# Kernel tuning notes

Hardware: AMD Instinct MI355X
Metric: run time of the kernel (lower is better)

## Reference

```python
import math
import jax, jax.numpy as jnp
import numpy as np

N_HEADS = 16


def setup_inputs() -> dict:
    key = jax.random.key(0)
    k1, k2 = jax.random.split(key)
    # qkv: [N, H*C, T] queries; y: [N, H*C, S] keys/values (k = v = y)
    qkv = jax.random.normal(k1, (2, 1024, 2048), dtype=jnp.float32)
    y = jax.random.normal(k2, (2, 1024, 2048), dtype=jnp.float32)
    return {"qkv": qkv, "y": y}


def reference(qkv, y):
    bs, width, length = qkv.shape
    ch = width // N_HEADS  # head dim = 64
    q = qkv.reshape(bs * N_HEADS, ch, length)          # [B*H, C, T]
    k = v = y.reshape(bs * N_HEADS, ch, -1)            # [B*H, C, S]
    scale = 1.0 / math.sqrt(math.sqrt(ch))             # applied to both q and k
    weight = jnp.einsum('bct,bcs->bts', q * scale, k * scale)  # [B*H, T, S]
    weight = jax.nn.softmax(weight.astype(jnp.float32), axis=-1).astype(weight.dtype)
    a = jnp.einsum('bts,bcs->bct', weight, v)          # [B*H, C, T]
    return a.reshape(bs, -1, length)                   # [N, H*C, T]
```

## Files before the change

kernel.cpp:

```cpp
#include <hip/hip_runtime.h>
#include <hip/hip_bf16.h>


typedef __attribute__((ext_vector_type(4))) float f32x4;
typedef __attribute__((ext_vector_type(8))) short bf16x8;
typedef __attribute__((ext_vector_type(4))) float float4_t;
typedef __attribute__((ext_vector_type(4))) unsigned u32x4;

__device__ __forceinline__ unsigned short f2bf(float f) {
  unsigned u = __builtin_bit_cast(unsigned, f);
  u += 0x7FFFu + ((u >> 16) & 1u);
  return (unsigned short)(u >> 16);
}

__device__ __forceinline__ float exp2_fast(float x) {
  float r;
  asm("v_exp_f32 %0, %1" : "=v"(r) : "v"(x));
  return r;
}

__device__ __forceinline__ unsigned cvt_pk_bf16(float a, float b) {
  unsigned r;
  asm("v_cvt_pk_bf16_f32 %0, %1, %2" : "=v"(r) : "v"(a), "v"(b));
  return r;
}

#define GLOAD_LDS16(g, l) __builtin_amdgcn_global_load_lds(                 \
    (const __attribute__((address_space(1))) unsigned*)(g),                 \
    (__attribute__((address_space(3))) unsigned*)(l), 16, 0, 0)

#define SCL (0.35355339059327373f * 1.2011224087864498f)

__global__ __launch_bounds__(256)
void prep(const float* __restrict__ qkv, const float* __restrict__ y,
          unsigned short* __restrict__ kT, unsigned short* __restrict__ v,
          unsigned short* __restrict__ qT) {
  __shared__ unsigned short tb[64][66];
  const int tid = threadIdx.x;
  const int isQ = blockIdx.x >> 10;
  const int b2  = blockIdx.x & 1023;
  const int bh  = b2 >> 5;
  const int s0  = (b2 & 31) * 64;
  const float* src = (isQ ? qkv : y) + (size_t)bh * 131072;

  const int c = tid >> 2, j = tid & 3;
  float fv[16];
  #pragma unroll
  for (int p = 0; p < 4; ++p) {
    float4_t a = *(const float4_t*)(src + c * 2048 + s0 + j * 16 + p * 4);
    #pragma unroll
    for (int i = 0; i < 4; ++i) fv[p * 4 + i] = a[i];
  }
  if (!isQ) {
    bf16x8 u0, u1;
    #pragma unroll
    for (int i = 0; i < 8; ++i) { u0[i] = (short)f2bf(fv[i]); u1[i] = (short)f2bf(fv[8 + i]); }
    unsigned short* vp = v + (size_t)bh * 131072 + c * 2048 + s0 + j * 16;
    *(bf16x8*)(vp) = u0;
    *(bf16x8*)(vp + 8) = u1;
  }
  #pragma unroll
  for (int m = 0; m < 8; ++m) {
    unsigned lo = f2bf(fv[2 * m] * SCL);
    unsigned hi = f2bf(fv[2 * m + 1] * SCL);
    *(unsigned*)&tb[c][j * 16 + 2 * m] = lo | (hi << 16);
  }
  __syncthreads();

  const int srow = tid >> 2, i2 = tid & 3;
  unsigned short outv[16];
  #pragma unroll
  for (int m = 0; m < 16; ++m) outv[m] = tb[i2 * 16 + m][srow];
  unsigned short* dT = (isQ ? qT : kT) + (size_t)bh * 131072 +
                       (size_t)(s0 + srow) * 64 + i2 * 16;
  *(bf16x8*)(dT)     = *(bf16x8*)&outv[0];
  *(bf16x8*)(dT + 8) = *(bf16x8*)&outv[8];
}

#define WBS 32768

__global__ __launch_bounds__(512, 2)
void attn_main(const unsigned short* __restrict__ kT,
               const unsigned short* __restrict__ v,
               const unsigned short* __restrict__ qT,
               float* __restrict__ out) {
  __shared__ __align__(16) char smem[2 * WBS];
  const int tid  = threadIdx.x;
  const int lane = tid & 63;
  const int w    = tid >> 6;
  const int c15  = lane & 15;
  const int g    = lane >> 4;

  const int bid = blockIdx.x;
  const int bh  = (bid & 7) * 4 + ((bid >> 3) & 3);
  const int t0  = (bid >> 5) * 256;

  const unsigned short* kg = kT + (size_t)bh * 131072;
  const unsigned short* vg = v  + (size_t)bh * 131072;
  float*                og = out + (size_t)bh * 131072;

  bf16x8 qf[2][2];
  {
    const unsigned short* qp0 = qT + (size_t)bh * 131072 +
                                (size_t)(t0 + w * 32 + c15) * 64 + 8 * g;
    qf[0][0] = *(const bf16x8*)(qp0);
    qf[0][1] = *(const bf16x8*)(qp0 + 32);
    qf[1][0] = *(const bf16x8*)(qp0 + 1024);
    qf[1][1] = *(const bf16x8*)(qp0 + 1024 + 32);
  }

  const int sr = tid >> 3, sb = tid & 7;
  const int ss = sb ^ (sr & 7);
  const unsigned short* kbase = kg + sr * 64 + ss * 8;
  const unsigned short* vbase = vg + sr * 2048 + ss * 8;
  char* const slds = smem + tid * 16;

  f32x4 oacc[2][4];
  #pragma unroll
  for (int tg = 0; tg < 2; ++tg)
    #pragma unroll
    for (int nc = 0; nc < 4; ++nc) oacc[tg][nc] = (f32x4){0.f, 0.f, 0.f, 0.f};
  float lsum[2] = {0.f, 0.f};

  auto QK = [&](f32x4 (&acc)[2][4], char* kb) {
    #pragma unroll
    for (int kt = 0; kt < 2; ++kt)
      #pragma unroll
      for (int nt = 0; nt < 4; ++nt) {
        const int srow = nt * 16 + c15;
        bf16x8 kf = *(bf16x8*)(kb + srow * 128 + (((kt * 4 + g) ^ (srow & 7)) * 16));
        acc[0][nt] = __builtin_amdgcn_mfma_f32_16x16x32_bf16(kf, qf[0][kt], acc[0][nt], 0, 0, 0);
        acc[1][nt] = __builtin_amdgcn_mfma_f32_16x16x32_bf16(kf, qf[1][kt], acc[1][nt], 0, 0, 0);
      }
  };
  auto SM = [&](f32x4 (&acc)[2][4], bf16x8 (&pa)[2][2]) {
    #pragma unroll
    for (int tg = 0; tg < 2; ++tg) {
      unsigned W[8];
      #pragma unroll
      for (int nt = 0; nt < 4; ++nt) {
        float p0 = exp2_fast(acc[tg][nt][0]);
        float p1 = exp2_fast(acc[tg][nt][1]);
        float p2 = exp2_fast(acc[tg][nt][2]);
        float p3 = exp2_fast(acc[tg][nt][3]);
        lsum[tg] += (p0 + p1) + (p2 + p3);
        W[nt * 2]     = cvt_pk_bf16(p0, p1);
        W[nt * 2 + 1] = cvt_pk_bf16(p2, p3);
      }
      #pragma unroll
      for (int kt = 0; kt < 2; ++kt) {
        unsigned a0 = W[kt * 4 + 0], b0 = W[kt * 4 + 2];
        unsigned a1 = W[kt * 4 + 1], b1 = W[kt * 4 + 3];
        asm volatile("v_permlane32_swap_b32 %0, %1" : "+v"(a0), "+v"(b0));
        asm volatile("v_permlane32_swap_b32 %0, %1" : "+v"(a1), "+v"(b1));
        asm volatile("v_permlane16_swap_b32 %0, %1" : "+v"(a0), "+v"(b0));
        asm volatile("v_permlane16_swap_b32 %0, %1" : "+v"(a1), "+v"(b1));
        u32x4 fw = {a0, a1, b0, b1};
        pa[tg][kt] = __builtin_bit_cast(bf16x8, fw);
      }
    }
  };
  auto PV = [&](bf16x8 (&pa)[2][2], char* vb) {
    #pragma unroll
    for (int kt = 0; kt < 2; ++kt)
      #pragma unroll
      for (int nc = 0; nc < 4; ++nc) {
        const int crow = nc * 16 + c15;
        bf16x8 vf = *(bf16x8*)(vb + crow * 128 + (((kt * 4 + g) ^ (crow & 7)) * 16));
        oacc[0][nc] = __builtin_amdgcn_mfma_f32_16x16x32_bf16(vf, pa[0][kt], oacc[0][nc], 0, 0, 0);
        oacc[1][nc] = __builtin_amdgcn_mfma_f32_16x16x32_bf16(vf, pa[1][kt], oacc[1][nc], 0, 0, 0);
      }
  };

  auto window = [&](int bs, int wn, bool doIssue) {
    asm volatile("s_waitcnt vmcnt(0)" ::: "memory");
    __builtin_amdgcn_s_barrier();
    __builtin_amdgcn_sched_barrier(0);
    if (doIssue) {
      const unsigned short* kp = kbase + (size_t)(wn + 1) * 8192;
      const unsigned short* vp = vbase + (wn + 1) * 128;
      char* const ob = slds + (bs ^ 1) * WBS;
      GLOAD_LDS16(kp,        ob);
      GLOAD_LDS16(kp + 4096, ob + 8192);
      GLOAD_LDS16(vp,        ob + 16384);
      GLOAD_LDS16(vp + 64,   ob + 24576);
    }
    __builtin_amdgcn_sched_barrier(0);

    char* const base = smem + bs * WBS;
    f32x4 accA[2][4], accB[2][4];
    #pragma unroll
    for (int tg = 0; tg < 2; ++tg)
      #pragma unroll
      for (int nt = 0; nt < 4; ++nt) {
        accA[tg][nt] = (f32x4){0.f, 0.f, 0.f, 0.f};
        accB[tg][nt] = (f32x4){0.f, 0.f, 0.f, 0.f};
      }
    __builtin_amdgcn_s_setprio(1);
    QK(accA, base);
    QK(accB, base + 8192);
    __builtin_amdgcn_s_setprio(0);
    bf16x8 paA[2][2], paB[2][2];
    SM(accA, paA);
    __builtin_amdgcn_s_setprio(1);
    PV(paA, base + 16384);
    __builtin_amdgcn_s_setprio(0);
    SM(accB, paB);
    __builtin_amdgcn_s_setprio(1);
    PV(paB, base + 24576);
    __builtin_amdgcn_s_setprio(0);
  };

  GLOAD_LDS16(kbase,        slds);
  GLOAD_LDS16(kbase + 4096, slds + 8192);
  GLOAD_LDS16(vbase,        slds + 16384);
  GLOAD_LDS16(vbase + 64,   slds + 24576);

  #pragma unroll 1
  for (int mi = 0; mi < 8; ++mi) {
    window(0, 2 * mi,     true);
    window(1, 2 * mi + 1, mi < 7);
  }

  #pragma unroll
  for (int tg = 0; tg < 2; ++tg) {
    lsum[tg] += __shfl_xor(lsum[tg], 16);
    lsum[tg] += __shfl_xor(lsum[tg], 32);
  }
  const float invl0 = 1.0f / lsum[0];
  const float invl1 = 1.0f / lsum[1];

  float* ob = og + t0 + w * 32 + c15 + (size_t)(4 * g) * 2048;
  #pragma unroll
  for (int nc = 0; nc < 4; ++nc)
    #pragma unroll
    for (int r = 0; r < 4; ++r) {
      ob[(size_t)(nc * 16 + r) * 2048]      = oacc[0][nc][r] * invl0;
      ob[(size_t)(nc * 16 + r) * 2048 + 16] = oacc[1][nc][r] * invl1;
    }
}

#define LDS_K 0
#define LDS_V 8192
#define LDS_P 16384
#define LDS_TOTAL 27648

__global__ __launch_bounds__(256)
void attn_fwd(const float* __restrict__ qkv, const float* __restrict__ y,
              float* __restrict__ out) {
  __shared__ __align__(16) char smem[LDS_TOTAL];
  const int tid  = threadIdx.x;
  const int lane = tid & 63;
  const int w    = tid >> 6;
  const int c15  = lane & 15;
  const int g    = lane >> 4;
  const int bh = blockIdx.x >> 5;
  const int t0 = (blockIdx.x & 31) * 64;
  const float* qg = qkv + (size_t)bh * 64 * 2048;
  const float* kg = y   + (size_t)bh * 64 * 2048;
  float*       og = out + (size_t)bh * 64 * 2048;
  const float SC = 0.35355339059327373f;
  typedef __attribute__((ext_vector_type(4))) float f4;
  bf16x8 qf[2];
  {
    const int tq = t0 + w * 16 + c15;
    #pragma unroll
    for (int kt = 0; kt < 2; ++kt)
      #pragma unroll
      for (int j = 0; j < 8; ++j)
        qf[kt][j] = (short)f2bf(qg[(kt * 32 + 8 * g + j) * 2048 + tq] * SC);
  }
  f32x4 oacc[4];
  #pragma unroll
  for (int nc = 0; nc < 4; ++nc) oacc[nc] = (f32x4){0.f, 0.f, 0.f, 0.f};
  float m_run[4], l_run[4];
  #pragma unroll
  for (int r = 0; r < 4; ++r) { m_run[r] = -1e30f; l_run[r] = 0.f; }
  const int ks_row = tid & 63, ks_cb = tid >> 6;
  const int vs_c = tid >> 2, vs_j = tid & 3;
  for (int it = 0; it < 32; ++it) {
    const int s0 = it * 64;
    #pragma unroll
    for (int pass = 0; pass < 2; ++pass) {
      const int cblk = pass * 4 + ks_cb;
      bf16x8 pk;
      #pragma unroll
      for (int i = 0; i < 8; ++i)
        pk[i] = (short)f2bf(kg[(cblk * 8 + i) * 2048 + s0 + ks_row] * SC);
      *(bf16x8*)(smem + LDS_K + ks_row * 128 + ((cblk ^ (ks_row & 7)) * 16)) = pk;
    }
    #pragma unroll
    for (int pass = 0; pass < 2; ++pass) {
      const int sblk = pass * 4 + vs_j;
      const f4 a = *(const f4*)(kg + vs_c * 2048 + s0 + sblk * 8);
      const f4 b = *(const f4*)(kg + vs_c * 2048 + s0 + sblk * 8 + 4);
      bf16x8 pv;
      #pragma unroll
      for (int i = 0; i < 4; ++i) { pv[i] = (short)f2bf(a[i]); pv[4 + i] = (short)f2bf(b[i]); }
      *(bf16x8*)(smem + LDS_V + vs_c * 128 + ((sblk ^ (vs_c & 7)) * 16)) = pv;
    }
    __syncthreads();
    f32x4 accs[4];
    #pragma unroll
    for (int nt = 0; nt < 4; ++nt) accs[nt] = (f32x4){0.f, 0.f, 0.f, 0.f};
    #pragma unroll
    for (int kt = 0; kt < 2; ++kt)
      #pragma unroll
      for (int nt = 0; nt < 4; ++nt) {
        const int srow = nt * 16 + c15;
        bf16x8 kf = *(bf16x8*)(smem + LDS_K + srow * 128 +
                               (((kt * 4 + g) ^ (srow & 7)) * 16));
        accs[nt] = __builtin_amdgcn_mfma_f32_16x16x32_bf16(qf[kt], kf, accs[nt], 0, 0, 0);
      }
    float mt[4];
    #pragma unroll
    for (int r = 0; r < 4; ++r)
      mt[r] = fmaxf(fmaxf(accs[0][r], accs[1][r]), fmaxf(accs[2][r], accs[3][r]));
    #pragma unroll
    for (int off = 1; off <= 8; off <<= 1)
      #pragma unroll
      for (int r = 0; r < 4; ++r) mt[r] = fmaxf(mt[r], __shfl_xor(mt[r], off));
    float alpha[4];
    #pragma unroll
    for (int r = 0; r < 4; ++r) {
      float mn = fmaxf(m_run[r], mt[r]);
      alpha[r] = __expf(m_run[r] - mn);
      m_run[r] = mn;
    }
    float ls[4] = {0.f, 0.f, 0.f, 0.f};
    #pragma unroll
    for (int nt = 0; nt < 4; ++nt)
      #pragma unroll
      for (int r = 0; r < 4; ++r) {
        float p = __expf(accs[nt][r] - m_run[r]);
        accs[nt][r] = p;
        ls[r] += p;
      }
    #pragma unroll
    for (int off = 1; off <= 8; off <<= 1)
      #pragma unroll
      for (int r = 0; r < 4; ++r) ls[r] += __shfl_xor(ls[r], off);
    #pragma unroll
    for (int r = 0; r < 4; ++r) l_run[r] = l_run[r] * alpha[r] + ls[r];
    #pragma unroll
    for (int nc = 0; nc < 4; ++nc)
      #pragma unroll
      for (int r = 0; r < 4; ++r) oacc[nc][r] *= alpha[r];
    char* pb = smem + LDS_P + w * 2816;
    #pragma unroll
    for (int nt = 0; nt < 4; ++nt)
      #pragma unroll
      for (int r = 0; r < 4; ++r)
        *(unsigned short*)(pb + (4 * g + r) * 176 + (nt * 16 + c15) * 2) =
            f2bf(accs[nt][r]);
    __builtin_amdgcn_sched_barrier(0);
    #pragma unroll
    for (int kt = 0; kt < 2; ++kt) {
      bf16x8 pf = *(bf16x8*)(pb + c15 * 176 + (kt * 32 + 8 * g) * 2);
      #pragma unroll
      for (int nc = 0; nc < 4; ++nc) {
        const int crow = nc * 16 + c15;
        bf16x8 vf = *(bf16x8*)(smem + LDS_V + crow * 128 +
                               (((kt * 4 + g) ^ (crow & 7)) * 16));
        oacc[nc] = __builtin_amdgcn_mfma_f32_16x16x32_bf16(pf, vf, oacc[nc], 0, 0, 0);
      }
    }
    __syncthreads();
  }
  float inv_l[4];
  #pragma unroll
  for (int r = 0; r < 4; ++r) inv_l[r] = 1.0f / l_run[r];
  float* ep = (float*)smem;
  #pragma unroll
  for (int nc = 0; nc < 4; ++nc)
    #pragma unroll
    for (int r = 0; r < 4; ++r)
      ep[(nc * 16 + c15) * 68 + (w * 16 + 4 * g + r)] = oacc[nc][r] * inv_l[r];
  __syncthreads();
  #pragma unroll
  for (int itr = 0; itr < 4; ++itr) {
    int idx = itr * 256 + tid;
    int cc  = idx >> 4;
    int v4  = idx & 15;
    f4 o = *(f4*)(ep + cc * 68 + v4 * 4);
    *(f4*)(og + cc * 2048 + t0 + v4 * 4) = o;
  }
}

extern "C" void kernel_launch(void* const* d_in, const int* in_sizes, int n_in,
                              void* d_out, int out_size, void* d_ws, size_t ws_size,
                              hipStream_t stream) {
  const float* qkv = (const float*)d_in[0];
  const float* y   = (const float*)d_in[1];
  float*       out = (float*)d_out;
  if (ws_size < (size_t)25165824) {
    attn_fwd<<<dim3(1024), dim3(256), 0, stream>>>(qkv, y, out);
    return;
  }
  unsigned short* kT = (unsigned short*)d_ws;
  unsigned short* vv = kT + 4194304;
  unsigned short* qT = kT + 8388608;
  prep<<<dim3(2048), dim3(256), 0, stream>>>(qkv, y, kT, vv, qT);
  attn_main<<<dim3(256), dim3(512), 0, stream>>>(kT, vv, qT, out);
}
```

Baseline: 53.49 us.

## Split KV window across wave halves with 64-query tiles and LDS reduction

```diff
diff --git a/kernel.cpp b/kernel.cpp
--- a/kernel.cpp
+++ b/kernel.cpp
@@ -78,18 +78,24 @@
 }
 
 #define WBS 32768
+#define EP_STR 66
+#define EP_W2  16896
+#define LSUM_OFF 67584
+#define SMEM_SZ 69632
 
 __global__ __launch_bounds__(512, 2)
 void attn_main(const unsigned short* __restrict__ kT,
                const unsigned short* __restrict__ v,
                const unsigned short* __restrict__ qT,
                float* __restrict__ out) {
-  __shared__ __align__(16) char smem[2 * WBS];
+  __shared__ __align__(16) char smem[SMEM_SZ];
   const int tid  = threadIdx.x;
   const int lane = tid & 63;
   const int w    = tid >> 6;
   const int c15  = lane & 15;
   const int g    = lane >> 4;
+  const int sh   = w >> 2;
+  const int w2   = w & 3;
 
   const int bid = blockIdx.x;
   const int bh  = (bid & 7) * 4 + ((bid >> 3) & 3);
@@ -99,14 +105,15 @@
   const unsigned short* vg = v  + (size_t)bh * 131072;
   float*                og = out + (size_t)bh * 131072;
 
-  bf16x8 qf[2][2];
+  bf16x8 qf[4][2];
   {
     const unsigned short* qp0 = qT + (size_t)bh * 131072 +
-                                (size_t)(t0 + w * 32 + c15) * 64 + 8 * g;
-    qf[0][0] = *(const bf16x8*)(qp0);
-    qf[0][1] = *(const bf16x8*)(qp0 + 32);
-    qf[1][0] = *(const bf16x8*)(qp0 + 1024);
-    qf[1][1] = *(const bf16x8*)(qp0 + 1024 + 32);
+                                (size_t)(t0 + w2 * 64 + c15) * 64 + 8 * g;
+    #pragma unroll
+    for (int tg = 0; tg < 4; ++tg) {
+      qf[tg][0] = *(const bf16x8*)(qp0 + tg * 1024);
+      qf[tg][1] = *(const bf16x8*)(qp0 + tg * 1024 + 32);
+    }
   }
 
   const int sr = tid >> 3, sb = tid & 7;
@@ -115,30 +122,31 @@
   const unsigned short* vbase = vg + sr * 2048 + ss * 8;
   char* const slds = smem + tid * 16;
 
-  f32x4 oacc[2][4];
-  #pragma unroll
-  for (int tg = 0; tg < 2; ++tg)
+  f32x4 oacc[4][4];
+  #pragma unroll
+  for (int tg = 0; tg < 4; ++tg)
     #pragma unroll
     for (int nc = 0; nc < 4; ++nc) oacc[tg][nc] = (f32x4){0.f, 0.f, 0.f, 0.f};
-  float lsum[2] = {0.f, 0.f};
-
-  auto QK = [&](f32x4 (&acc)[2][4], char* kb) {
+  float lsum[4] = {0.f, 0.f, 0.f, 0.f};
+
+  auto QK = [&](f32x4 (&acc)[4][2], char* kb) {
     #pragma unroll
     for (int kt = 0; kt < 2; ++kt)
       #pragma unroll
-      for (int nt = 0; nt < 4; ++nt) {
-        const int srow = nt * 16 + c15;
+      for (int nt = 0; nt < 2; ++nt) {
+        const int srow = sh * 32 + nt * 16 + c15;
         bf16x8 kf = *(bf16x8*)(kb + srow * 128 + (((kt * 4 + g) ^ (srow & 7)) * 16));
-        acc[0][nt] = __builtin_amdgcn_mfma_f32_16x16x32_bf16(kf, qf[0][kt], acc[0][nt], 0, 0, 0);
-        acc[1][nt] = __builtin_amdgcn_mfma_f32_16x16x32_bf16(kf, qf[1][kt], acc[1][nt], 0, 0, 0);
+        #pragma unroll
+        for (int tg = 0; tg < 4; ++tg)
+          acc[tg][nt] = __builtin_amdgcn_mfma_f32_16x16x32_bf16(kf, qf[tg][kt], acc[tg][nt], 0, 0, 0);
       }
   };
-  auto SM = [&](f32x4 (&acc)[2][4], bf16x8 (&pa)[2][2]) {
-    #pragma unroll
-    for (int tg = 0; tg < 2; ++tg) {
-      unsigned W[8];
-      #pragma unroll
-      for (int nt = 0; nt < 4; ++nt) {
+  auto SM = [&](f32x4 (&acc)[4][2], bf16x8 (&pa)[4]) {
+    #pragma unroll
+    for (int tg = 0; tg < 4; ++tg) {
+      unsigned W[4];
+      #pragma unroll
+      for (int nt = 0; nt < 2; ++nt) {
         float p0 = exp2_fast(acc[tg][nt][0]);
         float p1 = exp2_fast(acc[tg][nt][1]);
         float p2 = exp2_fast(acc[tg][nt][2]);
@@ -147,29 +155,24 @@
         W[nt * 2]     = cvt_pk_bf16(p0, p1);
         W[nt * 2 + 1] = cvt_pk_bf16(p2, p3);
       }
-      #pragma unroll
-      for (int kt = 0; kt < 2; ++kt) {
-        unsigned a0 = W[kt * 4 + 0], b0 = W[kt * 4 + 2];
-        unsigned a1 = W[kt * 4 + 1], b1 = W[kt * 4 + 3];
-        asm volatile("v_permlane32_swap_b32 %0, %1" : "+v"(a0), "+v"(b0));
-        asm volatile("v_permlane32_swap_b32 %0, %1" : "+v"(a1), "+v"(b1));
-        asm volatile("v_permlane16_swap_b32 %0, %1" : "+v"(a0), "+v"(b0));
-        asm volatile("v_permlane16_swap_b32 %0, %1" : "+v"(a1), "+v"(b1));
-        u32x4 fw = {a0, a1, b0, b1};
-        pa[tg][kt] = __builtin_bit_cast(bf16x8, fw);
-      }
+      unsigned a0 = W[0], b0 = W[2], a1 = W[1], b1 = W[3];
+      asm volatile("v_permlane32_swap_b32 %0, %1" : "+v"(a0), "+v"(b0));
+      asm volatile("v_permlane32_swap_b32 %0, %1" : "+v"(a1), "+v"(b1));
+      asm volatile("v_permlane16_swap_b32 %0, %1" : "+v"(a0), "+v"(b0));
+      asm volatile("v_permlane16_swap_b32 %0, %1" : "+v"(a1), "+v"(b1));
+      u32x4 fw = {a0, a1, b0, b1};
+      pa[tg] = __builtin_bit_cast(bf16x8, fw);
     }
   };
-  auto PV = [&](bf16x8 (&pa)[2][2], char* vb) {
-    #pragma unroll
-    for (int kt = 0; kt < 2; ++kt)
-      #pragma unroll
-      for (int nc = 0; nc < 4; ++nc) {
-        const int crow = nc * 16 + c15;
-        bf16x8 vf = *(bf16x8*)(vb + crow * 128 + (((kt * 4 + g) ^ (crow & 7)) * 16));
-        oacc[0][nc] = __builtin_amdgcn_mfma_f32_16x16x32_bf16(vf, pa[0][kt], oacc[0][nc], 0, 0, 0);
-        oacc[1][nc] = __builtin_amdgcn_mfma_f32_16x16x32_bf16(vf, pa[1][kt], oacc[1][nc], 0, 0, 0);
-      }
+  auto PV = [&](bf16x8 (&pa)[4], char* vb) {
+    #pragma unroll
+    for (int nc = 0; nc < 4; ++nc) {
+      const int crow = nc * 16 + c15;
+      bf16x8 vf = *(bf16x8*)(vb + crow * 128 + (((sh * 4 + g) ^ (crow & 7)) * 16));
+      #pragma unroll
+      for (int tg = 0; tg < 4; ++tg)
+        oacc[tg][nc] = __builtin_amdgcn_mfma_f32_16x16x32_bf16(vf, pa[tg], oacc[tg][nc], 0, 0, 0);
+    }
   };
 
   auto window = [&](int bs, int wn, bool doIssue) {
@@ -188,11 +191,11 @@
     __builtin_amdgcn_sched_barrier(0);
 
     char* const base = smem + bs * WBS;
-    f32x4 accA[2][4], accB[2][4];
-    #pragma unroll
-    for (int tg = 0; tg < 2; ++tg)
-      #pragma unroll
-      for (int nt = 0; nt < 4; ++nt) {
+    f32x4 accA[4][2], accB[4][2];
+    #pragma unroll
+    for (int tg = 0; tg < 4; ++tg)
+      #pragma unroll
+      for (int nt = 0; nt < 2; ++nt) {
         accA[tg][nt] = (f32x4){0.f, 0.f, 0.f, 0.f};
         accB[tg][nt] = (f32x4){0.f, 0.f, 0.f, 0.f};
       }
@@ -200,7 +203,7 @@
     QK(accA, base);
     QK(accB, base + 8192);
     __builtin_amdgcn_s_setprio(0);
-    bf16x8 paA[2][2], paB[2][2];
+    bf16x8 paA[4], paB[4];
     SM(accA, paA);
     __builtin_amdgcn_s_setprio(1);
     PV(paA, base + 16384);
@@ -223,21 +226,44 @@
   }
 
   #pragma unroll
-  for (int tg = 0; tg < 2; ++tg) {
+  for (int tg = 0; tg < 4; ++tg) {
     lsum[tg] += __shfl_xor(lsum[tg], 16);
     lsum[tg] += __shfl_xor(lsum[tg], 32);
   }
-  const float invl0 = 1.0f / lsum[0];
-  const float invl1 = 1.0f / lsum[1];
-
-  float* ob = og + t0 + w * 32 + c15 + (size_t)(4 * g) * 2048;
-  #pragma unroll
-  for (int nc = 0; nc < 4; ++nc)
-    #pragma unroll
-    for (int r = 0; r < 4; ++r) {
-      ob[(size_t)(nc * 16 + r) * 2048]      = oacc[0][nc][r] * invl0;
-      ob[(size_t)(nc * 16 + r) * 2048 + 16] = oacc[1][nc][r] * invl1;
-    }
+
+  __syncthreads();
+  float* lsl = (float*)(smem + LSUM_OFF);
+  if (lane < 16)
+    #pragma unroll
+    for (int tg = 0; tg < 4; ++tg) lsl[(w * 4 + tg) * 16 + c15] = lsum[tg];
+  if (sh == 0) {
+    float* ep = (float*)(smem + w2 * EP_W2);
+    #pragma unroll
+    for (int tg = 0; tg < 4; ++tg)
+      #pragma unroll
+      for (int nc = 0; nc < 4; ++nc)
+        #pragma unroll
+        for (int r = 0; r < 4; ++r)
+          ep[(nc * 16 + 4 * g + r) * EP_STR + tg * 16 + c15] = oacc[tg][nc][r];
+  }
+  __syncthreads();
+  if (sh == 1) {
+    float invl[4];
+    #pragma unroll
+    for (int tg = 0; tg < 4; ++tg)
+      invl[tg] = 1.0f / (lsum[tg] + lsl[(w2 * 4 + tg) * 16 + c15]);
+    float* ep = (float*)(smem + w2 * EP_W2);
+    float* ob = og + t0 + w2 * 64 + c15 + (size_t)(4 * g) * 2048;
+    #pragma unroll
+    for (int tg = 0; tg < 4; ++tg)
+      #pragma unroll
+      for (int nc = 0; nc < 4; ++nc)
+        #pragma unroll
+        for (int r = 0; r < 4; ++r) {
+          float o = ep[(nc * 16 + 4 * g + r) * EP_STR + tg * 16 + c15] + oacc[tg][nc][r];
+          ob[(size_t)(nc * 16 + r) * 2048 + tg * 16] = o * invl[tg];
+        }
+  }
 }
 
 #define LDS_K 0
```

Measured after the change: 54.40 us. No clear change (+1.7%).

## Software-pipeline QK of next window with softmax/PV of previous window

Applied to the files above, without the earlier changes.

```diff
diff --git a/kernel.cpp b/kernel.cpp
--- a/kernel.cpp
+++ b/kernel.cpp
@@ -77,14 +77,17 @@
   *(bf16x8*)(dT + 8) = *(bf16x8*)&outv[8];
 }
 
-#define WBS 32768
-
-__global__ __launch_bounds__(512, 2)
+#define KB0 0
+#define KB1 16384
+#define VR  32768
+#define SMEM_SZ 81920
+
+__global__ __launch_bounds__(512, 1)
 void attn_main(const unsigned short* __restrict__ kT,
                const unsigned short* __restrict__ v,
                const unsigned short* __restrict__ qT,
                float* __restrict__ out) {
-  __shared__ __align__(16) char smem[2 * WBS];
+  __shared__ __align__(16) char smem[SMEM_SZ];
   const int tid  = threadIdx.x;
   const int lane = tid & 63;
   const int w    = tid >> 6;
@@ -172,55 +175,79 @@
       }
   };
 
-  auto window = [&](int bs, int wn, bool doIssue) {
+  auto QK2 = [&](f32x4 (&aA)[2][4], f32x4 (&aB)[2][4], char* kb) {
+    #pragma unroll
+    for (int tg = 0; tg < 2; ++tg)
+      #pragma unroll
+      for (int nt = 0; nt < 4; ++nt) {
+        aA[tg][nt] = (f32x4){0.f, 0.f, 0.f, 0.f};
+        aB[tg][nt] = (f32x4){0.f, 0.f, 0.f, 0.f};
+      }
+    __builtin_amdgcn_s_setprio(1);
+    QK(aA, kb);
+    QK(aB, kb + 8192);
+    __builtin_amdgcn_s_setprio(0);
+  };
+  auto SMPV2 = [&](f32x4 (&aA)[2][4], f32x4 (&aB)[2][4], char* vb) {
+    bf16x8 paA[2][2], paB[2][2];
+    SM(aA, paA);
+    __builtin_amdgcn_s_setprio(1);
+    PV(paA, vb);
+    __builtin_amdgcn_s_setprio(0);
+    SM(aB, paB);
+    __builtin_amdgcn_s_setprio(1);
+    PV(paB, vb + 8192);
+    __builtin_amdgcn_s_setprio(0);
+  };
+
+  auto headIssue = [&](int wn, int vnxt_off) {
     asm volatile("s_waitcnt vmcnt(0)" ::: "memory");
     __builtin_amdgcn_s_barrier();
     __builtin_amdgcn_sched_barrier(0);
-    if (doIssue) {
+    if (wn + 1 < 16) {
       const unsigned short* kp = kbase + (size_t)(wn + 1) * 8192;
       const unsigned short* vp = vbase + (wn + 1) * 128;
-      char* const ob = slds + (bs ^ 1) * WBS;
-      GLOAD_LDS16(kp,        ob);
-      GLOAD_LDS16(kp + 4096, ob + 8192);
-      GLOAD_LDS16(vp,        ob + 16384);
-      GLOAD_LDS16(vp + 64,   ob + 24576);
+      char* kb = slds + (((wn + 1) & 1) ? KB1 : KB0);
+      char* vb = slds + vnxt_off;
+      GLOAD_LDS16(kp,        kb);
+      GLOAD_LDS16(kp + 4096, kb + 8192);
+      GLOAD_LDS16(vp,        vb);
+      GLOAD_LDS16(vp + 64,   vb + 8192);
     }
     __builtin_amdgcn_sched_barrier(0);
-
-    char* const base = smem + bs * WBS;
-    f32x4 accA[2][4], accB[2][4];
-    #pragma unroll
-    for (int tg = 0; tg < 2; ++tg)
-      #pragma unroll
-      for (int nt = 0; nt < 4; ++nt) {
-        accA[tg][nt] = (f32x4){0.f, 0.f, 0.f, 0.f};
-        accB[tg][nt] = (f32x4){0.f, 0.f, 0.f, 0.f};
-      }
-    __builtin_amdgcn_s_setprio(1);
-    QK(accA, base);
-    QK(accB, base + 8192);
-    __builtin_amdgcn_s_setprio(0);
-    bf16x8 paA[2][2], paB[2][2];
-    SM(accA, paA);
-    __builtin_amdgcn_s_setprio(1);
-    PV(paA, base + 16384);
-    __builtin_amdgcn_s_setprio(0);
-    SM(accB, paB);
-    __builtin_amdgcn_s_setprio(1);
-    PV(paB, base + 24576);
-    __builtin_amdgcn_s_setprio(0);
-  };
-
-  GLOAD_LDS16(kbase,        slds);
-  GLOAD_LDS16(kbase + 4096, slds + 8192);
-  GLOAD_LDS16(vbase,        slds + 16384);
-  GLOAD_LDS16(vbase + 64,   slds + 24576);
+  };
+
+  f32x4 aPA[2][4], aPB[2][4], aQA[2][4], aQB[2][4];
+
+  int vprv = VR + 32768, vcur = VR, vnxt = VR + 16384;
+  auto rot = [&]() { int t = vprv; vprv = vcur; vcur = vnxt; vnxt = t; };
+
+  GLOAD_LDS16(kbase,        slds + KB0);
+  GLOAD_LDS16(kbase + 4096, slds + KB0 + 8192);
+  GLOAD_LDS16(vbase,        slds + VR);
+  GLOAD_LDS16(vbase + 64,   slds + VR + 8192);
+
+  headIssue(0, vnxt);
+  QK2(aPA, aPB, smem + KB0);
+  rot();
 
   #pragma unroll 1
-  for (int mi = 0; mi < 8; ++mi) {
-    window(0, 2 * mi,     true);
-    window(1, 2 * mi + 1, mi < 7);
-  }
+  for (int mi = 0; mi < 7; ++mi) {
+    const int m = 2 * mi + 1;
+    headIssue(m, vnxt);
+    QK2(aQA, aQB, smem + KB1);
+    SMPV2(aPA, aPB, smem + vprv);
+    rot();
+    headIssue(m + 1, vnxt);
+    QK2(aPA, aPB, smem + KB0);
+    SMPV2(aQA, aQB, smem + vprv);
+    rot();
+  }
+
+  headIssue(15, vnxt);
+  QK2(aQA, aQB, smem + KB1);
+  SMPV2(aPA, aPB, smem + vprv);
+  SMPV2(aQA, aQB, smem + vcur);
 
   #pragma unroll
   for (int tg = 0; tg < 2; ++tg) {
```

After: 54.47 us. Within noise of the previous version (+1.8%).
